# Optimization experiments

Measured on AMD Instinct MI355X. Metric: run time of the kernel, lower is better.

The kernel has to match this reference:

```python
import jax, jax.numpy as jnp
import numpy as np

K_NN = 4  # hard-coded k in get_graph_feature(x, k=4)


def _conv1(h, Wm, s, b):
    # 1x1 conv1d + folded-BN (scale/shift) + ReLU
    return jax.nn.relu(jnp.einsum('oc,bcn->bon', Wm, h) * s[:, None] + b[:, None])


def _conv2(h, Wm, s, b):
    # 1x1 conv2d + folded-BN + ReLU
    return jax.nn.relu(jnp.einsum('oc,bcnk->bonk', Wm, h) * s[:, None, None] + b[:, None, None])


def _forward(x, W_dup, s_dup, b_dup, W_c1, s_c1, b_c1,
             W2a, s2a, b2a, W2b, s2b, b2b, W2c, s2c, b2c,
             W3a, s3a, b3a, W3b, s3b, b3b, W4a, bias4a, W4b, bias4b):
    B = x.shape[0]
    h = _conv1(x, W_dup, s_dup, b_dup)           # (B,256,1024)
    h = h.reshape(B, 128, 2048)                  # duplicate points: (B,128,2048)
    h = _conv1(h, W_c1, s_c1, b_c1)              # (B,64,2048)
    g = jnp.max(h, axis=2, keepdims=True)        # max_pool1d over all 2048 -> (B,64,1)
    # knn on 64-d features: pairwise = -||xi-xj||^2, topk picks nearest (self included)
    xx = jnp.sum(h * h, axis=1, keepdims=True)   # (B,1,P)
    inner = -2.0 * jnp.einsum('bcn,bcm->bnm', h, h)
    pd = -xx - inner - jnp.swapaxes(xx, 1, 2)    # (B,P,P)
    idx = jax.lax.top_k(pd, K_NN)[1]             # (B,P,k)
    xt = jnp.swapaxes(h, 1, 2)                   # (B,P,C)
    nb = xt[jnp.arange(B)[:, None, None], idx]   # gather neighbors: (B,P,k,C)
    ctr = xt[:, :, None, :]
    feat = jnp.concatenate([nb - ctr, jnp.broadcast_to(ctr, nb.shape)], axis=-1)  # (B,P,k,2C)
    feat = jnp.transpose(feat, (0, 3, 1, 2))     # (B,128,P,k)
    feat = _conv2(feat, W2a, s2a, b2a)
    feat = _conv2(feat, W2b, s2b, b2b)
    feat = _conv2(feat, W2c, s2c, b2c)           # (B,64,P,k)
    local = jnp.max(feat, axis=3)                # max over k -> (B,64,P)
    g = _conv1(g, W3a, s3a, b3a)
    g = _conv1(g, W3b, s3b, b3b)                 # (B,128,1)
    final = jnp.concatenate([local, jnp.broadcast_to(g, (B, 128, local.shape[2]))], axis=1)  # (B,192,P)
    h4 = jax.nn.relu(jnp.einsum('oc,bcn->bon', W4a, final) + bias4a[:, None])  # (B,256,P)
    out = jnp.einsum('oc,bcn->bon', W4b, h4) + bias4b[:, None]                 # (B,3,P)
    return out


def setup_inputs() -> dict:
    key = jax.random.key(0)
    ks = list(jax.random.split(key, 30))
    W = lambda k, o, c: jax.random.normal(k, (o, c), jnp.float32) * 0.05
    sc = lambda k, c: 1.0 + 0.1 * jax.random.normal(k, (c,), jnp.float32)
    bs = lambda k, c: 0.1 * jax.random.normal(k, (c,), jnp.float32)
    return {
        'search_keypoint': jax.random.normal(ks[0], (8, 128, 1024), jnp.float32),
        'W_dup': W(ks[1], 256, 128), 's_dup': sc(ks[2], 256), 'b_dup': bs(ks[3], 256),
        'W_c1': W(ks[4], 64, 128), 's_c1': sc(ks[5], 64), 'b_c1': bs(ks[6], 64),
        'W2a': W(ks[7], 64, 128), 's2a': sc(ks[8], 64), 'b2a': bs(ks[9], 64),
        'W2b': W(ks[10], 64, 64), 's2b': sc(ks[11], 64), 'b2b': bs(ks[12], 64),
        'W2c': W(ks[13], 64, 64), 's2c': sc(ks[14], 64), 'b2c': bs(ks[15], 64),
        'W3a': W(ks[16], 128, 64), 's3a': sc(ks[17], 128), 'b3a': bs(ks[18], 128),
        'W3b': W(ks[19], 128, 128), 's3b': sc(ks[20], 128), 'b3b': bs(ks[21], 128),
        'W4a': W(ks[22], 256, 192), 'bias4a': bs(ks[23], 256),
        'W4b': W(ks[24], 3, 256), 'bias4b': bs(ks[25], 3),
    }


def reference(search_keypoint, W_dup, s_dup, b_dup, W_c1, s_c1, b_c1,
              W2a, s2a, b2a, W2b, s2b, b2b, W2c, s2c, b2c,
              W3a, s3a, b3a, W3b, s3b, b3b, W4a, bias4a, W4b, bias4b):
    return _forward(search_keypoint, W_dup, s_dup, b_dup, W_c1, s_c1, b_c1,
                    W2a, s2a, b2a, W2b, s2b, b2b, W2c, s2c, b2c,
                    W3a, s3a, b3a, W3b, s3b, b3b, W4a, bias4a, W4b, bias4b)
```

## Files before the change

kernel.cpp:

```cpp
#include <hip/hip_runtime.h>
#include <float.h>

typedef __attribute__((ext_vector_type(8))) short short8;
typedef __attribute__((ext_vector_type(4))) float f32x4;
typedef unsigned short u16;
typedef unsigned long long u64;

static constexpr size_t OFF_W     = 0;
static constexpr size_t OFF_YZ    = 131072;
static constexpr size_t OFF_Zf    = 1179648;
static constexpr size_t OFF_FEATR = 2228224;
static constexpr size_t OFF_FIN   = 6422528;
static constexpr size_t OFF_XX    = 9568256;
static constexpr size_t OFF_G     = 9584640;
static constexpr size_t OFF_G3BS  = 9617408;
static constexpr size_t WS_FLOATS = 9652736;

static constexpr size_t WO_DUP = 0;
static constexpr size_t WO_C1  = 32768;
static constexpr size_t WO_2A  = 40960;
static constexpr size_t WO_2B  = 49152;
static constexpr size_t WO_2C  = 53248;
static constexpr size_t WO_4A  = 57344;

__device__ __forceinline__ void gl_lds16(const void* g, void* l) {
    __builtin_amdgcn_global_load_lds(
        (const __attribute__((address_space(1))) void*)g,
        (__attribute__((address_space(3))) void*)l, 16, 0, 0);
}

__device__ __forceinline__ u16 f2bf(float x) {
    union { float f; unsigned int u; } v; v.f = x;
    unsigned int r = v.u + 0x7fffu + ((v.u >> 16) & 1u);
    return (u16)(r >> 16);
}
__device__ __forceinline__ float bf2f(u16 h) {
    union { unsigned int u; float f; } v; v.u = ((unsigned int)h) << 16;
    return v.f;
}
__device__ __forceinline__ void split2(float x, u16& h, u16& l) {
    h = f2bf(x);
    l = f2bf(x - bf2f(h));
}

__device__ __forceinline__ unsigned int fmap(float f) {
    unsigned int u = __float_as_uint(f);
    return u ^ ((unsigned int)((int)u >> 31) | 0x80000000u);
}
__device__ __forceinline__ u64 mkkey(float f, int m) {
    return ((u64)fmap(f) << 32) | (unsigned int)(2047 - m);
}
static __device__ __forceinline__ void ins4k(u64 k, u64 bk[4])
{
#pragma unroll
    for (int s = 0; s < 4; ++s) {
        bool better = k > bk[s];
        u64 t = bk[s];
        bk[s] = better ? k : bk[s];
        k = better ? t : k;
    }
}

__global__ __launch_bounds__(256) void wsplit(
    const float* W_dup, const float* W_c1, const float* W2a,
    const float* W2b, const float* W2c, const float* W4a,
    u16* whi, u16* wlo)
{
    int t = blockIdx.x * 256 + threadIdx.x;
    float v;
    if      (t < 40960) v = (t < 32768) ? W_dup[t] : W_c1[t - 32768];
    else if (t < 53248) v = (t < 49152) ? W2a[t - 40960] : W2b[t - 49152];
    else                v = (t < 57344) ? W2c[t - 53248] : W4a[t - 57344];
    u16 h, l; split2(v, h, l);
    whi[t] = h; wlo[t] = l;
}

__global__ __launch_bounds__(256) void tsplit_x(const float* x, u16* xthi, u16* xtlo)
{
    const int b = blockIdx.z, c0 = blockIdx.y * 64, n0 = blockIdx.x * 64;
    const int t = threadIdx.x;
    __shared__ float tile[64][65];
    const float* xb = x + ((size_t)b * 128 + c0) * 1024;
#pragma unroll
    for (int i = 0; i < 16; ++i) {
        int c = i * 4 + (t >> 6), n = t & 63;
        tile[c][n] = xb[(size_t)c * 1024 + n0 + n];
    }
    __syncthreads();
#pragma unroll
    for (int i = 0; i < 16; ++i) {
        int n = i * 4 + (t >> 6), c = t & 63;
        u16 h, l; split2(tile[c][n], h, l);
        const size_t o = ((size_t)b * 1024 + n0 + n) * 128 + c0 + c;
        xthi[o] = h; xtlo[o] = l;
    }
}

__global__ __launch_bounds__(256) void backbone(
    const u16* __restrict__ xthi, const u16* __restrict__ xtlo,
    const u16* __restrict__ whi, const u16* __restrict__ wlo,
    const float* __restrict__ s_dup, const float* __restrict__ b_dup,
    const float* __restrict__ s_c1, const float* __restrict__ b_c1,
    u16* __restrict__ h2thi, u16* __restrict__ h2tlo,
    float* __restrict__ xxb, float* __restrict__ gp,
    float* __restrict__ y, float* __restrict__ z)
{
    const int t = threadIdx.x;
    const int wu = t >> 6;
    const int lane = t & 63;
    const int j = lane & 15, q = lane >> 4;
    const int nb = blockIdx.x;
    const int b  = blockIdx.y;
    const int n0 = nb * 16;

    __shared__ __align__(16) u16 h1h[32 * 136], h1l[32 * 136];
    __shared__ __align__(16) u16 h2h[32 * 72],  h2l[32 * 72];
    __shared__ float xxp[2][2][16];
    __shared__ float gpart[2][64];

    {
        const size_t arow = ((size_t)b * 1024 + n0 + j) * 128;
        short8 ahv[4], alv[4];
#pragma unroll
        for (int ks = 0; ks < 4; ++ks) {
            ahv[ks] = *(const short8*)(xthi + arow + q * 8 + ks * 32);
            alv[ks] = *(const short8*)(xtlo + arow + q * 8 + ks * 32);
        }
        const u16* wdh = whi + WO_DUP;
        const u16* wdl = wlo + WO_DUP;
#pragma unroll
        for (int ci = 0; ci < 4; ++ci) {
            const int o = (wu * 4 + ci) * 16 + j;
            f32x4 acc = (f32x4){0.f, 0.f, 0.f, 0.f};
#pragma unroll
            for (int ks = 0; ks < 4; ++ks) {
                short8 bh = *(const short8*)(wdh + (size_t)o * 128 + q * 8 + ks * 32);
                short8 bl = *(const short8*)(wdl + (size_t)o * 128 + q * 8 + ks * 32);
                acc = __builtin_amdgcn_mfma_f32_16x16x32_bf16(ahv[ks], bh, acc, 0, 0, 0);
                acc = __builtin_amdgcn_mfma_f32_16x16x32_bf16(ahv[ks], bl, acc, 0, 0, 0);
                acc = __builtin_amdgcn_mfma_f32_16x16x32_bf16(alv[ks], bh, acc, 0, 0, 0);
            }
            const float sc = s_dup[o], bi = b_dup[o];
            const int lrbase = (j & 1) * 16;
            const int col = (wu * 4 + ci) * 8 + (j >> 1);
#pragma unroll
            for (int r = 0; r < 4; ++r) {
                float v = fmaxf(acc[r] * sc + bi, 0.f);
                u16 h, l; split2(v, h, l);
                const int lr = lrbase + q * 4 + r;
                h1h[lr * 136 + col] = h;
                h1l[lr * 136 + col] = l;
            }
        }
    }
    __syncthreads();

    {
        const int g = wu >> 1, ch = wu & 1;
        short8 ahv[4], alv[4];
#pragma unroll
        for (int ks = 0; ks < 4; ++ks) {
            ahv[ks] = *(const short8*)&h1h[(g * 16 + j) * 136 + q * 8 + ks * 32];
            alv[ks] = *(const short8*)&h1l[(g * 16 + j) * 136 + q * 8 + ks * 32];
        }
        const u16* wch = whi + WO_C1;
        const u16* wcl = wlo + WO_C1;
        float sq[4] = {0.f, 0.f, 0.f, 0.f};
        float cm[2];
#pragma unroll
        for (int ci = 0; ci < 2; ++ci) {
            const int o = (ch * 2 + ci) * 16 + j;
            f32x4 acc = (f32x4){0.f, 0.f, 0.f, 0.f};
#pragma unroll
            for (int ks = 0; ks < 4; ++ks) {
                short8 bh = *(const short8*)(wch + (size_t)o * 128 + q * 8 + ks * 32);
                short8 bl = *(const short8*)(wcl + (size_t)o * 128 + q * 8 + ks * 32);
                acc = __builtin_amdgcn_mfma_f32_16x16x32_bf16(ahv[ks], bh, acc, 0, 0, 0);
                acc = __builtin_amdgcn_mfma_f32_16x16x32_bf16(ahv[ks], bl, acc, 0, 0, 0);
                acc = __builtin_amdgcn_mfma_f32_16x16x32_bf16(alv[ks], bh, acc, 0, 0, 0);
            }
            const float sc = s_c1[o], bi = b_c1[o];
            float vmax = -FLT_MAX;
#pragma unroll
            for (int r = 0; r < 4; ++r) {
                float v = fmaxf(acc[r] * sc + bi, 0.f);
                sq[r] += v * v;
                vmax = fmaxf(vmax, v);
                u16 h, l; split2(v, h, l);
                const size_t R = (size_t)b * 2048 + g * 1024 + n0 + q * 4 + r;
                h2thi[R * 64 + o] = h;
                h2tlo[R * 64 + o] = l;
                const int lr = g * 16 + q * 4 + r;
                h2h[lr * 72 + o] = h;
                h2l[lr * 72 + o] = l;
            }
            cm[ci] = vmax;
        }
#pragma unroll
        for (int r = 0; r < 4; ++r) {
#pragma unroll
            for (int mask = 1; mask < 16; mask <<= 1)
                sq[r] += __shfl_xor(sq[r], mask, 64);
        }
        if (j == 0) {
#pragma unroll
            for (int r = 0; r < 4; ++r) xxp[g][ch][q * 4 + r] = sq[r];
        }
#pragma unroll
        for (int ci = 0; ci < 2; ++ci) {
            cm[ci] = fmaxf(cm[ci], __shfl_xor(cm[ci], 16, 64));
            cm[ci] = fmaxf(cm[ci], __shfl_xor(cm[ci], 32, 64));
        }
        if (q == 0) {
#pragma unroll
            for (int ci = 0; ci < 2; ++ci)
                gpart[g][(ch * 2 + ci) * 16 + j] = cm[ci];
        }
    }
    __syncthreads();

    if (t < 32) {
        const int g = t >> 4, i = t & 15;
        xxb[(size_t)b * 2048 + g * 1024 + n0 + i] = xxp[g][0][i] + xxp[g][1][i];
    }
    if (t >= 64 && t < 128) {
        const int c = t - 64;
        gp[((size_t)b * 64 + nb) * 64 + c] = fmaxf(gpart[0][c], gpart[1][c]);
    }

    {
        const int g = wu & 1, half = wu >> 1;
        short8 ahv[2], alv[2];
#pragma unroll
        for (int ks = 0; ks < 2; ++ks) {
            ahv[ks] = *(const short8*)&h2h[(g * 16 + j) * 72 + q * 8 + ks * 32];
            alv[ks] = *(const short8*)&h2l[(g * 16 + j) * 72 + q * 8 + ks * 32];
        }
        const u16* w2h = whi + WO_2A;
        const u16* w2l = wlo + WO_2A;
        float* dst = half ? z : y;
#pragma unroll
        for (int ci = 0; ci < 4; ++ci) {
            const int o = ci * 16 + j;
            f32x4 acc = (f32x4){0.f, 0.f, 0.f, 0.f};
#pragma unroll
            for (int ks = 0; ks < 2; ++ks) {
                short8 bh = *(const short8*)(w2h + (size_t)o * 128 + half * 64 + q * 8 + ks * 32);
                short8 bl = *(const short8*)(w2l + (size_t)o * 128 + half * 64 + q * 8 + ks * 32);
                acc = __builtin_amdgcn_mfma_f32_16x16x32_bf16(ahv[ks], bh, acc, 0, 0, 0);
                acc = __builtin_amdgcn_mfma_f32_16x16x32_bf16(ahv[ks], bl, acc, 0, 0, 0);
                acc = __builtin_amdgcn_mfma_f32_16x16x32_bf16(alv[ks], bh, acc, 0, 0, 0);
            }
#pragma unroll
            for (int r = 0; r < 4; ++r) {
                const size_t R = (size_t)b * 2048 + g * 1024 + n0 + q * 4 + r;
                dst[R * 64 + o] = acc[r];
            }
        }
    }
}

struct __align__(16) KBuf {
    u16 hi[4096];
    u16 lo[4096];
    float xm[64];
};

__global__ __launch_bounds__(256) void knn_topk(const u16* __restrict__ thi,
                                                const u16* __restrict__ tlo,
                                                const float* __restrict__ xx,
                                                u64* __restrict__ part)
{
    const int b    = blockIdx.z;
    const int mh   = blockIdx.y;
    const int t    = threadIdx.x;
    const int wu   = __builtin_amdgcn_readfirstlane(t >> 6);
    const int lane = t & 63;
    const int j    = lane & 15;
    const int q    = lane >> 4;
    const int nrow0 = blockIdx.x * 64 + wu * 16;

    const u16* th = thi + (size_t)b * 2048 * 64;
    const u16* tl = tlo + (size_t)b * 2048 * 64;
    const float* xb = xx + (size_t)b * 2048;

    __shared__ KBuf sb[2];

    const size_t arow = (size_t)(nrow0 + j) * 64;
    short8 ah0 = *(const short8*)(th + arow + q * 8);
    short8 ah1 = *(const short8*)(th + arow + 32 + q * 8);
    short8 al0 = *(const short8*)(tl + arow + q * 8);
    short8 al1 = *(const short8*)(tl + arow + 32 + q * 8);

    u64 bk[4][4];
#pragma unroll
    for (int r = 0; r < 4; ++r)
#pragma unroll
        for (int s = 0; s < 4; ++s) bk[r][s] = 0ull;

    const int mbeg = mh * 1024;

#define KNN_STAGE(BUF, M0)                                                        \
    {                                                                             \
        const u16* sh = th + (size_t)((M0) + lane) * 64;                          \
        const u16* sl = tl + (size_t)((M0) + lane) * 64;                          \
        gl_lds16(sh + (2 * wu) * 8,     &sb[BUF].hi[(2 * wu) * 512]);             \
        gl_lds16(sh + (2 * wu + 1) * 8, &sb[BUF].hi[(2 * wu + 1) * 512]);         \
        gl_lds16(sl + (2 * wu) * 8,     &sb[BUF].lo[(2 * wu) * 512]);             \
        gl_lds16(sl + (2 * wu + 1) * 8, &sb[BUF].lo[(2 * wu + 1) * 512]);         \
        if (wu == 0 && lane < 16) gl_lds16(xb + (M0) + lane * 4, &sb[BUF].xm[0]); \
    }

    KNN_STAGE(0, mbeg)

    for (int tt = 0; tt < 16; ++tt) {
        __syncthreads();
        if (tt < 15) KNN_STAGE((tt + 1) & 1, mbeg + (tt + 1) * 64)
        const KBuf& bf = sb[tt & 1];
        const int m0 = mbeg + tt * 64;

        float pds[4][4];
#pragma unroll
        for (int sub = 0; sub < 4; ++sub) {
            const int ml = sub * 16 + j;
            short8 bh0 = *(const short8*)&bf.hi[(q) * 512 + ml * 8];
            short8 bh1 = *(const short8*)&bf.hi[(4 + q) * 512 + ml * 8];
            short8 bl0 = *(const short8*)&bf.lo[(q) * 512 + ml * 8];
            short8 bl1 = *(const short8*)&bf.lo[(4 + q) * 512 + ml * 8];
            const float xmv = bf.xm[ml];
            f32x4 accA = (f32x4){0.f, 0.f, 0.f, 0.f};
            f32x4 accB = (f32x4){0.f, 0.f, 0.f, 0.f};
            accA = __builtin_amdgcn_mfma_f32_16x16x32_bf16(ah0, bh0, accA, 0, 0, 0);
            accB = __builtin_amdgcn_mfma_f32_16x16x32_bf16(ah1, bh1, accB, 0, 0, 0);
            accA = __builtin_amdgcn_mfma_f32_16x16x32_bf16(ah0, bl0, accA, 0, 0, 0);
            accB = __builtin_amdgcn_mfma_f32_16x16x32_bf16(ah1, bl1, accB, 0, 0, 0);
            accA = __builtin_amdgcn_mfma_f32_16x16x32_bf16(al0, bh0, accA, 0, 0, 0);
            accB = __builtin_amdgcn_mfma_f32_16x16x32_bf16(al1, bh1, accB, 0, 0, 0);
            accA = __builtin_amdgcn_mfma_f32_16x16x32_bf16(al0, bl0, accA, 0, 0, 0);
            accB = __builtin_amdgcn_mfma_f32_16x16x32_bf16(al1, bl1, accB, 0, 0, 0);
#pragma unroll
            for (int r = 0; r < 4; ++r)
                pds[sub][r] = __builtin_fmaf(2.f, accA[r] + accB[r], -xmv);
        }

#pragma unroll
        for (int r = 0; r < 4; ++r) {
            float mx = fmaxf(fmaxf(pds[0][r], pds[1][r]), fmaxf(pds[2][r], pds[3][r]));
            if (fmap(mx) >= (unsigned int)(bk[r][3] >> 32)) {
#pragma unroll
                for (int sub = 0; sub < 4; ++sub) {
                    u64 key = mkkey(pds[sub][r], m0 + sub * 16 + j);
                    if (key > bk[r][3]) ins4k(key, bk[r]);
                }
            }
        }
    }
#undef KNN_STAGE

#pragma unroll
    for (int rr = 0; rr < 4; ++rr) {
#pragma unroll
        for (int mask = 1; mask < 16; mask <<= 1) {
            u64 pk[4];
#pragma unroll
            for (int s = 0; s < 4; ++s) pk[s] = __shfl_xor(bk[rr][s], mask, 64);
#pragma unroll
            for (int s = 0; s < 4; ++s) ins4k(pk[s], bk[rr]);
        }
    }
    if (j == 0) {
#pragma unroll
        for (int r = 0; r < 4; ++r) {
            const int nrow = nrow0 + q * 4 + r;
            u64* pp = part + (((size_t)b * 2 + mh) * 2048 + nrow) * 4;
            pp[0] = bk[r][0]; pp[1] = bk[r][1]; pp[2] = bk[r][2]; pp[3] = bk[r][3];
        }
    }
}

__global__ __launch_bounds__(128) void gconv_kernel(
    const float* __restrict__ gp,
    const float* __restrict__ W3a, const float* __restrict__ s3a, const float* __restrict__ b3a,
    const float* __restrict__ W3b, const float* __restrict__ s3b, const float* __restrict__ b3b,
    u16* __restrict__ g3bh, u16* __restrict__ g3bl)
{
    const int b = blockIdx.x;
    const int t = threadIdx.x;
    __shared__ float gl[64], ga[128];
    if (t < 64) {
        float m = -FLT_MAX;
        for (int s = 0; s < 64; ++s)
            m = fmaxf(m, gp[((size_t)b * 64 + s) * 64 + t]);
        gl[t] = m;
    }
    __syncthreads();
    float a = 0.f;
#pragma unroll
    for (int c = 0; c < 64; ++c) a += W3a[t * 64 + c] * gl[c];
    ga[t] = fmaxf(a * s3a[t] + b3a[t], 0.f);
    __syncthreads();
    float o = 0.f;
#pragma unroll
    for (int c = 0; c < 128; ++c) o += W3b[t * 128 + c] * ga[c];
    float v = fmaxf(o * s3b[t] + b3b[t], 0.f);
    u16 h, l; split2(v, h, l);
    g3bh[(size_t)b * 128 + t] = h;
    g3bl[(size_t)b * 128 + t] = l;
}

__global__ __launch_bounds__(64) void fused_edge(
    const u64* __restrict__ part,
    const float* __restrict__ y, const float* __restrict__ z,
    const float* __restrict__ s2a, const float* __restrict__ b2a,
    const u16* __restrict__ w2bh, const u16* __restrict__ w2bl,
    const float* __restrict__ s2b, const float* __restrict__ b2b,
    const u16* __restrict__ w2ch, const u16* __restrict__ w2cl,
    const float* __restrict__ s2c, const float* __restrict__ b2c,
    const u16* __restrict__ g3bh, const u16* __restrict__ g3bl,
    u16* __restrict__ finhi, u16* __restrict__ finlo)
{
    const int lane = threadIdx.x & 63;
    const int j = lane & 15, q = lane >> 4;
    const int gb = blockIdx.x;
    const int b = gb >> 9;
    const int n0 = (gb & 511) * 4;

    __shared__ __align__(16) u16 plh[16 * 72];
    __shared__ __align__(16) u16 pll[16 * 72];
    __shared__ int sidx[16];

    if (lane < 4) {
        const int n = n0 + lane;
        u64 fk[4] = {0ull, 0ull, 0ull, 0ull};
#pragma unroll
        for (int qt = 0; qt < 2; ++qt) {
            const u64* pp = part + (((size_t)b * 2 + qt) * 2048 + n) * 4;
#pragma unroll
            for (int s = 0; s < 4; ++s) ins4k(pp[s], fk);
        }
        int4 ii;
        ii.x = 2047 - (int)(fk[0] & 0x7ff);
        ii.y = 2047 - (int)(fk[1] & 0x7ff);
        ii.z = 2047 - (int)(fk[2] & 0x7ff);
        ii.w = 2047 - (int)(fk[3] & 0x7ff);
        *(int4*)&sidx[lane * 4] = ii;
    }

    {
        const int row = lane >> 2;
        const int c0 = (lane & 3) * 16;
        const int id = sidx[row];
        const int nfull = n0 + (row >> 2);
        const float* yb = y + (size_t)b * 2048 * 64;
        const float* yi = yb + (size_t)id * 64;
        const float* yn = yb + (size_t)nfull * 64;
        const float* zn = z + ((size_t)b * 2048 + nfull) * 64;
        u16* oh = &plh[row * 72 + c0];
        u16* ol = &pll[row * 72 + c0];
#pragma unroll
        for (int cc = 0; cc < 16; cc += 4) {
            const int c = c0 + cc;
            float4 a  = *(const float4*)(yi + c);
            float4 bq = *(const float4*)(yn + c);
            float4 cq = *(const float4*)(zn + c);
            float4 sv = *(const float4*)(s2a + c);
            float4 bb = *(const float4*)(b2a + c);
            float v0 = fmaxf((a.x - bq.x + cq.x) * sv.x + bb.x, 0.f);
            float v1 = fmaxf((a.y - bq.y + cq.y) * sv.y + bb.y, 0.f);
            float v2 = fmaxf((a.z - bq.z + cq.z) * sv.z + bb.z, 0.f);
            float v3 = fmaxf((a.w - bq.w + cq.w) * sv.w + bb.w, 0.f);
            union { u16 u[4]; uint2 v; } ph, pl;
            split2(v0, ph.u[0], pl.u[0]);
            split2(v1, ph.u[1], pl.u[1]);
            split2(v2, ph.u[2], pl.u[2]);
            split2(v3, ph.u[3], pl.u[3]);
            *(uint2*)(oh + cc) = ph.v;
            *(uint2*)(ol + cc) = pl.v;
        }
    }

    {
        const int abase = j * 72 + q * 8;
        short8 ah0 = *(const short8*)&plh[abase];
        short8 ah1 = *(const short8*)&plh[abase + 32];
        short8 al0 = *(const short8*)&pll[abase];
        short8 al1 = *(const short8*)&pll[abase + 32];
#pragma unroll
        for (int ct = 0; ct < 4; ++ct) {
            const int o = ct * 16 + j;
            short8 bh0 = *(const short8*)(w2bh + (size_t)o * 64 + q * 8);
            short8 bh1 = *(const short8*)(w2bh + (size_t)o * 64 + 32 + q * 8);
            short8 bl0 = *(const short8*)(w2bl + (size_t)o * 64 + q * 8);
            short8 bl1 = *(const short8*)(w2bl + (size_t)o * 64 + 32 + q * 8);
            f32x4 acc = (f32x4){0.f, 0.f, 0.f, 0.f};
            acc = __builtin_amdgcn_mfma_f32_16x16x32_bf16(ah0, bh0, acc, 0, 0, 0);
            acc = __builtin_amdgcn_mfma_f32_16x16x32_bf16(ah0, bl0, acc, 0, 0, 0);
            acc = __builtin_amdgcn_mfma_f32_16x16x32_bf16(al0, bh0, acc, 0, 0, 0);
            acc = __builtin_amdgcn_mfma_f32_16x16x32_bf16(ah1, bh1, acc, 0, 0, 0);
            acc = __builtin_amdgcn_mfma_f32_16x16x32_bf16(ah1, bl1, acc, 0, 0, 0);
            acc = __builtin_amdgcn_mfma_f32_16x16x32_bf16(al1, bh1, acc, 0, 0, 0);
            const float sc = s2b[o], bi = b2b[o];
#pragma unroll
            for (int r = 0; r < 4; ++r) {
                float v = fmaxf(acc[r] * sc + bi, 0.f);
                u16 h, l; split2(v, h, l);
                const int row = q * 4 + r;
                plh[row * 72 + o] = h;
                pll[row * 72 + o] = l;
            }
        }
    }

    {
        const int abase = j * 72 + q * 8;
        short8 ah0 = *(const short8*)&plh[abase];
        short8 ah1 = *(const short8*)&plh[abase + 32];
        short8 al0 = *(const short8*)&pll[abase];
        short8 al1 = *(const short8*)&pll[abase + 32];
        const size_t finrow = (size_t)b * 2048 + n0 + q;
#pragma unroll
        for (int ct = 0; ct < 4; ++ct) {
            const int o = ct * 16 + j;
            short8 bh0 = *(const short8*)(w2ch + (size_t)o * 64 + q * 8);
            short8 bh1 = *(const short8*)(w2ch + (size_t)o * 64 + 32 + q * 8);
            short8 bl0 = *(const short8*)(w2cl + (size_t)o * 64 + q * 8);
            short8 bl1 = *(const short8*)(w2cl + (size_t)o * 64 + 32 + q * 8);
            f32x4 acc = (f32x4){0.f, 0.f, 0.f, 0.f};
            acc = __builtin_amdgcn_mfma_f32_16x16x32_bf16(ah0, bh0, acc, 0, 0, 0);
            acc = __builtin_amdgcn_mfma_f32_16x16x32_bf16(ah0, bl0, acc, 0, 0, 0);
            acc = __builtin_amdgcn_mfma_f32_16x16x32_bf16(al0, bh0, acc, 0, 0, 0);
            acc = __builtin_amdgcn_mfma_f32_16x16x32_bf16(ah1, bh1, acc, 0, 0, 0);
            acc = __builtin_amdgcn_mfma_f32_16x16x32_bf16(ah1, bl1, acc, 0, 0, 0);
            acc = __builtin_amdgcn_mfma_f32_16x16x32_bf16(al1, bh1, acc, 0, 0, 0);
            const float sc = s2c[o], bi = b2c[o];
            float m = -FLT_MAX;
#pragma unroll
            for (int r = 0; r < 4; ++r)
                m = fmaxf(m, fmaxf(acc[r] * sc + bi, 0.f));
            u16 h, l; split2(m, h, l);
            finhi[finrow * 192 + o] = h;
            finlo[finrow * 192 + o] = l;
        }

        const int r = lane >> 4;
        const int chunk = lane & 15;
        const size_t br = (size_t)b * 2048 + n0 + r;
        short8 gh = *(const short8*)(g3bh + (size_t)b * 128 + chunk * 8);
        short8 glv = *(const short8*)(g3bl + (size_t)b * 128 + chunk * 8);
        *(short8*)(finhi + br * 192 + 64 + chunk * 8) = gh;
        *(short8*)(finlo + br * 192 + 64 + chunk * 8) = glv;
    }
}

__global__ __launch_bounds__(64) void conv_final(
    const u16* __restrict__ Whi, const u16* __restrict__ Wlo,
    const float* __restrict__ bias,
    const u16* __restrict__ Ahi, const u16* __restrict__ Alo,
    const float* __restrict__ W2, const float* __restrict__ bias2,
    float* __restrict__ out)
{
    const int lane = threadIdx.x & 63;
    const int j = lane & 15, q = lane >> 4;
    const int n0g = blockIdx.x * 16;

    short8 a_hi[6], a_lo[6];
    const u16* arow_h = Ahi + (size_t)(n0g + j) * 192 + q * 8;
    const u16* arow_l = Alo + (size_t)(n0g + j) * 192 + q * 8;
#pragma unroll
    for (int ks = 0; ks < 6; ++ks) {
        a_hi[ks] = *(const short8*)(arow_h + ks * 32);
        a_lo[ks] = *(const short8*)(arow_l + ks * 32);
    }

    float p[3][4];
#pragma unroll
    for (int oo = 0; oo < 3; ++oo)
#pragma unroll
        for (int r = 0; r < 4; ++r) p[oo][r] = 0.f;

#pragma unroll
    for (int ct = 0; ct < 16; ++ct) {
        const int o = ct * 16 + j;
        const u16* wr_h = Whi + (size_t)o * 192 + q * 8;
        const u16* wr_l = Wlo + (size_t)o * 192 + q * 8;
        f32x4 acc = (f32x4){0.f, 0.f, 0.f, 0.f};
#pragma unroll
        for (int ks = 0; ks < 6; ++ks) {
            short8 bh = *(const short8*)(wr_h + ks * 32);
            short8 bl = *(const short8*)(wr_l + ks * 32);
            acc = __builtin_amdgcn_mfma_f32_16x16x32_bf16(a_hi[ks], bh, acc, 0, 0, 0);
            acc = __builtin_amdgcn_mfma_f32_16x16x32_bf16(a_hi[ks], bl, acc, 0, 0, 0);
            acc = __builtin_amdgcn_mfma_f32_16x16x32_bf16(a_lo[ks], bh, acc, 0, 0, 0);
        }
        const float bi = bias[o];
        float w0 = W2[o], w1 = W2[256 + o], w2 = W2[512 + o];
#pragma unroll
        for (int r = 0; r < 4; ++r) {
            float v = fmaxf(acc[r] + bi, 0.f);
            p[0][r] += w0 * v;
            p[1][r] += w1 * v;
            p[2][r] += w2 * v;
        }
    }

#pragma unroll
    for (int oo = 0; oo < 3; ++oo)
#pragma unroll
        for (int r = 0; r < 4; ++r) {
#pragma unroll
            for (int mask = 1; mask < 16; mask <<= 1)
                p[oo][r] += __shfl_xor(p[oo][r], mask, 64);
        }
    if (j == 0) {
        const int row0 = n0g + q * 4;
        const int b = row0 >> 11;
#pragma unroll
        for (int r = 0; r < 4; ++r) {
            const int n = (row0 + r) & 2047;
#pragma unroll
            for (int oo = 0; oo < 3; ++oo)
                out[((size_t)b * 3 + oo) * 2048 + n] = p[oo][r] + bias2[oo];
        }
    }
}

extern "C" void kernel_launch(void* const* d_in, const int* in_sizes, int n_in,
                              void* d_out, int out_size, void* d_ws, size_t ws_size,
                              hipStream_t stream)
{
    const float* x     = (const float*)d_in[0];
    const float* W_dup = (const float*)d_in[1];
    const float* s_dup = (const float*)d_in[2];
    const float* b_dup = (const float*)d_in[3];
    const float* W_c1  = (const float*)d_in[4];
    const float* s_c1  = (const float*)d_in[5];
    const float* b_c1  = (const float*)d_in[6];
    const float* W2a   = (const float*)d_in[7];
    const float* s2a   = (const float*)d_in[8];
    const float* b2a   = (const float*)d_in[9];
    const float* W2b   = (const float*)d_in[10];
    const float* s2b   = (const float*)d_in[11];
    const float* b2b   = (const float*)d_in[12];
    const float* W2c   = (const float*)d_in[13];
    const float* s2c   = (const float*)d_in[14];
    const float* b2c   = (const float*)d_in[15];
    const float* W3a   = (const float*)d_in[16];
    const float* s3a   = (const float*)d_in[17];
    const float* b3a   = (const float*)d_in[18];
    const float* W3b   = (const float*)d_in[19];
    const float* s3b   = (const float*)d_in[20];
    const float* b3b   = (const float*)d_in[21];
    const float* W4a   = (const float*)d_in[22];
    const float* b4a   = (const float*)d_in[23];
    const float* W4b   = (const float*)d_in[24];
    const float* b4b   = (const float*)d_in[25];

    if (ws_size < WS_FLOATS * sizeof(float)) return;

    float* ws = (float*)d_ws;
    u16* whi   = (u16*)(ws + OFF_W);
    u16* wlo   = whi + 131072;
    u16* xthi  = (u16*)(ws + OFF_FEATR);
    u16* xtlo  = xthi + 1048576;
    u64* part  = (u64*)(ws + OFF_FEATR);
    float* y    = ws + OFF_YZ;
    float* z    = ws + OFF_Zf;
    u16* h2thi = (u16*)(ws + OFF_FIN);
    u16* h2tlo = h2thi + 1048576;
    u16* finhi  = (u16*)(ws + OFF_FIN);
    u16* finlo  = finhi + 3145728;
    float* xxb  = ws + OFF_XX;
    float* gp   = ws + OFF_G;
    u16* g3bh   = (u16*)(ws + OFF_G3BS);
    u16* g3bl   = g3bh + 1024;
    float* out  = (float*)d_out;

    wsplit<<<416, 256, 0, stream>>>(W_dup, W_c1, W2a, W2b, W2c, W4a, whi, wlo);
    tsplit_x<<<dim3(16, 2, 8), 256, 0, stream>>>(x, xthi, xtlo);
    backbone<<<dim3(64, 8), 256, 0, stream>>>(
        xthi, xtlo, whi, wlo, s_dup, b_dup, s_c1, b_c1,
        h2thi, h2tlo, xxb, gp, y, z);
    gconv_kernel<<<8, 128, 0, stream>>>(gp, W3a, s3a, b3a, W3b, s3b, b3b, g3bh, g3bl);
    knn_topk<<<dim3(32, 2, 8), 256, 0, stream>>>(h2thi, h2tlo, xxb, part);
    fused_edge<<<4096, 64, 0, stream>>>(
        part, y, z, s2a, b2a,
        whi + WO_2B, wlo + WO_2B, s2b, b2b,
        whi + WO_2C, wlo + WO_2C, s2c, b2c,
        g3bh, g3bl, finhi, finlo);
    conv_final<<<1024, 64, 0, stream>>>(
        whi + WO_4A, wlo + WO_4A, b4a, finhi, finlo, W4b, b4b, out);
}
```

Measured before the change: 261.1 us.

## Fold global feature into conv4a bias, merge prep kernels, widen backbone blocks

The 128-channel global feature is identical for every point, so its contribution through W4a is computed once per batch in gconv_kernel and added as a per-batch bias in conv_final. The final conv then uses only the 64 local channels, and fused_edge no longer writes the broadcast global columns, which removes most of the fin buffer traffic and two thirds of the conv_final MFMAs. The weight and input split kernels are merged into one launch, and backbone goes from 256 to 512 threads per block, splitting the channel tiles across 8 waves. The per-batch dot products in gconv run in plain fp32 on 8 blocks, which adds a small serial step.

```diff
diff --git a/kernel.cpp b/kernel.cpp
--- a/kernel.cpp
+++ b/kernel.cpp
@@ -13,7 +13,7 @@
 static constexpr size_t OFF_FIN   = 6422528;
 static constexpr size_t OFF_XX    = 9568256;
 static constexpr size_t OFF_G     = 9584640;
-static constexpr size_t OFF_G3BS  = 9617408;
+static constexpr size_t OFF_G4    = 9617408;
 static constexpr size_t WS_FLOATS = 9652736;
 
 static constexpr size_t WO_DUP = 0;
@@ -61,42 +61,47 @@
     }
 }
 
-__global__ __launch_bounds__(256) void wsplit(
-    const float* W_dup, const float* W_c1, const float* W2a,
-    const float* W2b, const float* W2c, const float* W4a,
-    u16* whi, u16* wlo)
-{
-    int t = blockIdx.x * 256 + threadIdx.x;
-    float v;
-    if      (t < 40960) v = (t < 32768) ? W_dup[t] : W_c1[t - 32768];
-    else if (t < 53248) v = (t < 49152) ? W2a[t - 40960] : W2b[t - 49152];
-    else                v = (t < 57344) ? W2c[t - 53248] : W4a[t - 57344];
-    u16 h, l; split2(v, h, l);
-    whi[t] = h; wlo[t] = l;
-}
-
-__global__ __launch_bounds__(256) void tsplit_x(const float* x, u16* xthi, u16* xtlo)
-{
-    const int b = blockIdx.z, c0 = blockIdx.y * 64, n0 = blockIdx.x * 64;
-    const int t = threadIdx.x;
+__global__ __launch_bounds__(256) void prep(
+    const float* __restrict__ W_dup, const float* __restrict__ W_c1,
+    const float* __restrict__ W2a, const float* __restrict__ W2b,
+    const float* __restrict__ W2c, const float* __restrict__ W4a,
+    const float* __restrict__ x,
+    u16* __restrict__ whi, u16* __restrict__ wlo,
+    u16* __restrict__ xthi, u16* __restrict__ xtlo)
+{
     __shared__ float tile[64][65];
-    const float* xb = x + ((size_t)b * 128 + c0) * 1024;
-#pragma unroll
-    for (int i = 0; i < 16; ++i) {
-        int c = i * 4 + (t >> 6), n = t & 63;
-        tile[c][n] = xb[(size_t)c * 1024 + n0 + n];
-    }
-    __syncthreads();
-#pragma unroll
-    for (int i = 0; i < 16; ++i) {
-        int n = i * 4 + (t >> 6), c = t & 63;
-        u16 h, l; split2(tile[c][n], h, l);
-        const size_t o = ((size_t)b * 1024 + n0 + n) * 128 + c0 + c;
-        xthi[o] = h; xtlo[o] = l;
-    }
-}
-
-__global__ __launch_bounds__(256) void backbone(
+    if (blockIdx.x < 416) {
+        int t = blockIdx.x * 256 + threadIdx.x;
+        float v;
+        if      (t < 40960) v = (t < 32768) ? W_dup[t] : W_c1[t - 32768];
+        else if (t < 53248) v = (t < 49152) ? W2a[t - 40960] : W2b[t - 49152];
+        else                v = (t < 57344) ? W2c[t - 53248] : W4a[t - 57344];
+        u16 h, l; split2(v, h, l);
+        whi[t] = h; wlo[t] = l;
+    } else {
+        const int bb = blockIdx.x - 416;
+        const int n0 = (bb & 15) * 64;
+        const int c0 = ((bb >> 4) & 1) * 64;
+        const int b  = bb >> 5;
+        const int t  = threadIdx.x;
+        const float* xb = x + ((size_t)b * 128 + c0) * 1024;
+#pragma unroll
+        for (int i = 0; i < 16; ++i) {
+            int c = i * 4 + (t >> 6), n = t & 63;
+            tile[c][n] = xb[(size_t)c * 1024 + n0 + n];
+        }
+        __syncthreads();
+#pragma unroll
+        for (int i = 0; i < 16; ++i) {
+            int n = i * 4 + (t >> 6), c = t & 63;
+            u16 h, l; split2(tile[c][n], h, l);
+            const size_t o = ((size_t)b * 1024 + n0 + n) * 128 + c0 + c;
+            xthi[o] = h; xtlo[o] = l;
+        }
+    }
+}
+
+__global__ __launch_bounds__(512) void backbone(
     const u16* __restrict__ xthi, const u16* __restrict__ xtlo,
     const u16* __restrict__ whi, const u16* __restrict__ wlo,
     const float* __restrict__ s_dup, const float* __restrict__ b_dup,
@@ -115,7 +120,7 @@
 
     __shared__ __align__(16) u16 h1h[32 * 136], h1l[32 * 136];
     __shared__ __align__(16) u16 h2h[32 * 72],  h2l[32 * 72];
-    __shared__ float xxp[2][2][16];
+    __shared__ float xxp[2][4][16];
     __shared__ float gpart[2][64];
 
     {
@@ -129,8 +134,9 @@
         const u16* wdh = whi + WO_DUP;
         const u16* wdl = wlo + WO_DUP;
 #pragma unroll
-        for (int ci = 0; ci < 4; ++ci) {
-            const int o = (wu * 4 + ci) * 16 + j;
+        for (int ci = 0; ci < 2; ++ci) {
+            const int ctile = wu * 2 + ci;
+            const int o = ctile * 16 + j;
             f32x4 acc = (f32x4){0.f, 0.f, 0.f, 0.f};
 #pragma unroll
             for (int ks = 0; ks < 4; ++ks) {
@@ -142,7 +148,7 @@
             }
             const float sc = s_dup[o], bi = b_dup[o];
             const int lrbase = (j & 1) * 16;
-            const int col = (wu * 4 + ci) * 8 + (j >> 1);
+            const int col = ctile * 8 + (j >> 1);
 #pragma unroll
             for (int r = 0; r < 4; ++r) {
                 float v = fmaxf(acc[r] * sc + bi, 0.f);
@@ -156,7 +162,7 @@
     __syncthreads();
 
     {
-        const int g = wu >> 1, ch = wu & 1;
+        const int g = wu >> 2, cq = wu & 3;
         short8 ahv[4], alv[4];
 #pragma unroll
         for (int ks = 0; ks < 4; ++ks) {
@@ -165,36 +171,31 @@
         }
         const u16* wch = whi + WO_C1;
         const u16* wcl = wlo + WO_C1;
-        float sq[4] = {0.f, 0.f, 0.f, 0.f};
-        float cm[2];
-#pragma unroll
-        for (int ci = 0; ci < 2; ++ci) {
-            const int o = (ch * 2 + ci) * 16 + j;
-            f32x4 acc = (f32x4){0.f, 0.f, 0.f, 0.f};
-#pragma unroll
-            for (int ks = 0; ks < 4; ++ks) {
-                short8 bh = *(const short8*)(wch + (size_t)o * 128 + q * 8 + ks * 32);
-                short8 bl = *(const short8*)(wcl + (size_t)o * 128 + q * 8 + ks * 32);
-                acc = __builtin_amdgcn_mfma_f32_16x16x32_bf16(ahv[ks], bh, acc, 0, 0, 0);
-                acc = __builtin_amdgcn_mfma_f32_16x16x32_bf16(ahv[ks], bl, acc, 0, 0, 0);
-                acc = __builtin_amdgcn_mfma_f32_16x16x32_bf16(alv[ks], bh, acc, 0, 0, 0);
-            }
-            const float sc = s_c1[o], bi = b_c1[o];
-            float vmax = -FLT_MAX;
-#pragma unroll
-            for (int r = 0; r < 4; ++r) {
-                float v = fmaxf(acc[r] * sc + bi, 0.f);
-                sq[r] += v * v;
-                vmax = fmaxf(vmax, v);
-                u16 h, l; split2(v, h, l);
-                const size_t R = (size_t)b * 2048 + g * 1024 + n0 + q * 4 + r;
-                h2thi[R * 64 + o] = h;
-                h2tlo[R * 64 + o] = l;
-                const int lr = g * 16 + q * 4 + r;
-                h2h[lr * 72 + o] = h;
-                h2l[lr * 72 + o] = l;
-            }
-            cm[ci] = vmax;
+        const int o = cq * 16 + j;
+        f32x4 acc = (f32x4){0.f, 0.f, 0.f, 0.f};
+#pragma unroll
+        for (int ks = 0; ks < 4; ++ks) {
+            short8 bh = *(const short8*)(wch + (size_t)o * 128 + q * 8 + ks * 32);
+            short8 bl = *(const short8*)(wcl + (size_t)o * 128 + q * 8 + ks * 32);
+            acc = __builtin_amdgcn_mfma_f32_16x16x32_bf16(ahv[ks], bh, acc, 0, 0, 0);
+            acc = __builtin_amdgcn_mfma_f32_16x16x32_bf16(ahv[ks], bl, acc, 0, 0, 0);
+            acc = __builtin_amdgcn_mfma_f32_16x16x32_bf16(alv[ks], bh, acc, 0, 0, 0);
+        }
+        const float sc = s_c1[o], bi = b_c1[o];
+        float sq[4];
+        float cm = -FLT_MAX;
+#pragma unroll
+        for (int r = 0; r < 4; ++r) {
+            float v = fmaxf(acc[r] * sc + bi, 0.f);
+            sq[r] = v * v;
+            cm = fmaxf(cm, v);
+            u16 h, l; split2(v, h, l);
+            const size_t R = (size_t)b * 2048 + g * 1024 + n0 + q * 4 + r;
+            h2thi[R * 64 + o] = h;
+            h2tlo[R * 64 + o] = l;
+            const int lr = g * 16 + q * 4 + r;
+            h2h[lr * 72 + o] = h;
+            h2l[lr * 72 + o] = l;
         }
 #pragma unroll
         for (int r = 0; r < 4; ++r) {
@@ -204,24 +205,18 @@
         }
         if (j == 0) {
 #pragma unroll
-            for (int r = 0; r < 4; ++r) xxp[g][ch][q * 4 + r] = sq[r];
-        }
-#pragma unroll
-        for (int ci = 0; ci < 2; ++ci) {
-            cm[ci] = fmaxf(cm[ci], __shfl_xor(cm[ci], 16, 64));
-            cm[ci] = fmaxf(cm[ci], __shfl_xor(cm[ci], 32, 64));
-        }
-        if (q == 0) {
-#pragma unroll
-            for (int ci = 0; ci < 2; ++ci)
-                gpart[g][(ch * 2 + ci) * 16 + j] = cm[ci];
-        }
+            for (int r = 0; r < 4; ++r) xxp[g][cq][q * 4 + r] = sq[r];
+        }
+        cm = fmaxf(cm, __shfl_xor(cm, 16, 64));
+        cm = fmaxf(cm, __shfl_xor(cm, 32, 64));
+        if (q == 0) gpart[g][cq * 16 + j] = cm;
     }
     __syncthreads();
 
     if (t < 32) {
         const int g = t >> 4, i = t & 15;
-        xxb[(size_t)b * 2048 + g * 1024 + n0 + i] = xxp[g][0][i] + xxp[g][1][i];
+        xxb[(size_t)b * 2048 + g * 1024 + n0 + i] =
+            (xxp[g][0][i] + xxp[g][1][i]) + (xxp[g][2][i] + xxp[g][3][i]);
     }
     if (t >= 64 && t < 128) {
         const int c = t - 64;
@@ -229,7 +224,7 @@
     }
 
     {
-        const int g = wu & 1, half = wu >> 1;
+        const int g = wu >> 2, half = (wu >> 1) & 1, cg = wu & 1;
         short8 ahv[2], alv[2];
 #pragma unroll
         for (int ks = 0; ks < 2; ++ks) {
@@ -240,8 +235,8 @@
         const u16* w2l = wlo + WO_2A;
         float* dst = half ? z : y;
 #pragma unroll
-        for (int ci = 0; ci < 4; ++ci) {
-            const int o = ci * 16 + j;
+        for (int ci = 0; ci < 2; ++ci) {
+            const int o = (cg * 2 + ci) * 16 + j;
             f32x4 acc = (f32x4){0.f, 0.f, 0.f, 0.f};
 #pragma unroll
             for (int ks = 0; ks < 2; ++ks) {
@@ -382,11 +377,11 @@
     const float* __restrict__ gp,
     const float* __restrict__ W3a, const float* __restrict__ s3a, const float* __restrict__ b3a,
     const float* __restrict__ W3b, const float* __restrict__ s3b, const float* __restrict__ b3b,
-    u16* __restrict__ g3bh, u16* __restrict__ g3bl)
+    const float* __restrict__ W4a, float* __restrict__ g4)
 {
     const int b = blockIdx.x;
     const int t = threadIdx.x;
-    __shared__ float gl[64], ga[128];
+    __shared__ float gl[64], ga[128], gb[128];
     if (t < 64) {
         float m = -FLT_MAX;
         for (int s = 0; s < 64; ++s)
@@ -402,10 +397,15 @@
     float o = 0.f;
 #pragma unroll
     for (int c = 0; c < 128; ++c) o += W3b[t * 128 + c] * ga[c];
-    float v = fmaxf(o * s3b[t] + b3b[t], 0.f);
-    u16 h, l; split2(v, h, l);
-    g3bh[(size_t)b * 128 + t] = h;
-    g3bl[(size_t)b * 128 + t] = l;
+    gb[t] = fmaxf(o * s3b[t] + b3b[t], 0.f);
+    __syncthreads();
+    for (int oo = t; oo < 256; oo += 128) {
+        float s = 0.f;
+#pragma unroll 4
+        for (int c = 0; c < 128; ++c)
+            s += W4a[(size_t)oo * 192 + 64 + c] * gb[c];
+        g4[(size_t)b * 256 + oo] = s;
+    }
 }
 
 __global__ __launch_bounds__(64) void fused_edge(
@@ -416,7 +416,6 @@
     const float* __restrict__ s2b, const float* __restrict__ b2b,
     const u16* __restrict__ w2ch, const u16* __restrict__ w2cl,
     const float* __restrict__ s2c, const float* __restrict__ b2c,
-    const u16* __restrict__ g3bh, const u16* __restrict__ g3bl,
     u16* __restrict__ finhi, u16* __restrict__ finlo)
 {
     const int lane = threadIdx.x & 63;
@@ -538,17 +537,9 @@
             for (int r = 0; r < 4; ++r)
                 m = fmaxf(m, fmaxf(acc[r] * sc + bi, 0.f));
             u16 h, l; split2(m, h, l);
-            finhi[finrow * 192 + o] = h;
-            finlo[finrow * 192 + o] = l;
-        }
-
-        const int r = lane >> 4;
-        const int chunk = lane & 15;
-        const size_t br = (size_t)b * 2048 + n0 + r;
-        short8 gh = *(const short8*)(g3bh + (size_t)b * 128 + chunk * 8);
-        short8 glv = *(const short8*)(g3bl + (size_t)b * 128 + chunk * 8);
-        *(short8*)(finhi + br * 192 + 64 + chunk * 8) = gh;
-        *(short8*)(finlo + br * 192 + 64 + chunk * 8) = glv;
+            finhi[finrow * 64 + o] = h;
+            finlo[finrow * 64 + o] = l;
+        }
     }
 }
 
@@ -556,18 +547,20 @@
     const u16* __restrict__ Whi, const u16* __restrict__ Wlo,
     const float* __restrict__ bias,
     const u16* __restrict__ Ahi, const u16* __restrict__ Alo,
+    const float* __restrict__ g4,
     const float* __restrict__ W2, const float* __restrict__ bias2,
     float* __restrict__ out)
 {
     const int lane = threadIdx.x & 63;
     const int j = lane & 15, q = lane >> 4;
     const int n0g = blockIdx.x * 16;
-
-    short8 a_hi[6], a_lo[6];
-    const u16* arow_h = Ahi + (size_t)(n0g + j) * 192 + q * 8;
-    const u16* arow_l = Alo + (size_t)(n0g + j) * 192 + q * 8;
-#pragma unroll
-    for (int ks = 0; ks < 6; ++ks) {
+    const int b = n0g >> 11;
+
+    short8 a_hi[2], a_lo[2];
+    const u16* arow_h = Ahi + (size_t)(n0g + j) * 64 + q * 8;
+    const u16* arow_l = Alo + (size_t)(n0g + j) * 64 + q * 8;
+#pragma unroll
+    for (int ks = 0; ks < 2; ++ks) {
         a_hi[ks] = *(const short8*)(arow_h + ks * 32);
         a_lo[ks] = *(const short8*)(arow_l + ks * 32);
     }
@@ -585,14 +578,14 @@
         const u16* wr_l = Wlo + (size_t)o * 192 + q * 8;
         f32x4 acc = (f32x4){0.f, 0.f, 0.f, 0.f};
 #pragma unroll
-        for (int ks = 0; ks < 6; ++ks) {
+        for (int ks = 0; ks < 2; ++ks) {
             short8 bh = *(const short8*)(wr_h + ks * 32);
             short8 bl = *(const short8*)(wr_l + ks * 32);
             acc = __builtin_amdgcn_mfma_f32_16x16x32_bf16(a_hi[ks], bh, acc, 0, 0, 0);
             acc = __builtin_amdgcn_mfma_f32_16x16x32_bf16(a_hi[ks], bl, acc, 0, 0, 0);
             acc = __builtin_amdgcn_mfma_f32_16x16x32_bf16(a_lo[ks], bh, acc, 0, 0, 0);
         }
-        const float bi = bias[o];
+        const float bi = bias[o] + g4[(size_t)b * 256 + o];
         float w0 = W2[o], w1 = W2[256 + o], w2 = W2[512 + o];
 #pragma unroll
         for (int r = 0; r < 4; ++r) {
@@ -613,7 +606,6 @@
         }
     if (j == 0) {
         const int row0 = n0g + q * 4;
-        const int b = row0 >> 11;
 #pragma unroll
         for (int r = 0; r < 4; ++r) {
             const int n = (row0 + r) & 2047;
@@ -668,25 +660,24 @@
     u16* h2thi = (u16*)(ws + OFF_FIN);
     u16* h2tlo = h2thi + 1048576;
     u16* finhi  = (u16*)(ws + OFF_FIN);
-    u16* finlo  = finhi + 3145728;
+    u16* finlo  = finhi + 1048576;
     float* xxb  = ws + OFF_XX;
     float* gp   = ws + OFF_G;
-    u16* g3bh   = (u16*)(ws + OFF_G3BS);
-    u16* g3bl   = g3bh + 1024;
+    float* g4   = ws + OFF_G4;
     float* out  = (float*)d_out;
 
-    wsplit<<<416, 256, 0, stream>>>(W_dup, W_c1, W2a, W2b, W2c, W4a, whi, wlo);
-    tsplit_x<<<dim3(16, 2, 8), 256, 0, stream>>>(x, xthi, xtlo);
-    backbone<<<dim3(64, 8), 256, 0, stream>>>(
+    prep<<<672, 256, 0, stream>>>(W_dup, W_c1, W2a, W2b, W2c, W4a, x,
+                                  whi, wlo, xthi, xtlo);
+    backbone<<<dim3(64, 8), 512, 0, stream>>>(
         xthi, xtlo, whi, wlo, s_dup, b_dup, s_c1, b_c1,
         h2thi, h2tlo, xxb, gp, y, z);
-    gconv_kernel<<<8, 128, 0, stream>>>(gp, W3a, s3a, b3a, W3b, s3b, b3b, g3bh, g3bl);
+    gconv_kernel<<<8, 128, 0, stream>>>(gp, W3a, s3a, b3a, W3b, s3b, b3b, W4a, g4);
     knn_topk<<<dim3(32, 2, 8), 256, 0, stream>>>(h2thi, h2tlo, xxb, part);
     fused_edge<<<4096, 64, 0, stream>>>(
         part, y, z, s2a, b2a,
         whi + WO_2B, wlo + WO_2B, s2b, b2b,
         whi + WO_2C, wlo + WO_2C, s2c, b2c,
-        g3bh, g3bl, finhi, finlo);
+        finhi, finlo);
     conv_final<<<1024, 64, 0, stream>>>(
-        whi + WO_4A, wlo + WO_4A, b4a, finhi, finlo, W4b, b4b, out);
-}
+        whi + WO_4A, wlo + WO_4A, b4a, finhi, finlo, g4, W4b, b4b, out);
+}
```

Result: faster. 244.7 us (-6.3%).
